# Performance work log

Measured on AMD Instinct MI355X. Metric: run time of the kernel, lower is better.

The kernel has to match this reference:

```python
import jax, jax.numpy as jnp
import numpy as np

BS, SLEN, EM = 32, 4096, 256


def setup_inputs() -> dict:
    key = jax.random.key(0)
    ks = jax.random.split(key, 8)
    word_embedded = jax.random.normal(ks[0], (BS, SLEN, EM), dtype=jnp.float32)
    # valid-token mask: first `length` tokens valid per row (True = keep)
    lengths = jax.random.randint(ks[1], (BS, 1), SLEN // 2, SLEN + 1)
    mask = jnp.arange(SLEN)[None, :] < lengths  # (BS, SLEN) bool
    s = 1.0 / np.sqrt(EM)
    w_query = jax.random.uniform(ks[2], (EM, 1), minval=-1.0, maxval=1.0, dtype=jnp.float32)  # Linear(1, em, bias=False)
    wq = jax.random.uniform(ks[3], (EM, EM), minval=-s, maxval=s, dtype=jnp.float32)
    bq = jax.random.uniform(ks[4], (EM,), minval=-s, maxval=s, dtype=jnp.float32)
    wk = jax.random.uniform(ks[5], (EM, EM), minval=-s, maxval=s, dtype=jnp.float32)
    bk = jax.random.uniform(ks[6], (EM,), minval=-s, maxval=s, dtype=jnp.float32)
    se = 1.0 / np.sqrt(2 * EM)
    we = jax.random.uniform(ks[7], (1, 2 * EM), minval=-se, maxval=se, dtype=jnp.float32)
    be = jnp.zeros((1,), dtype=jnp.float32)
    return {"word_embedded": word_embedded, "mask": mask, "w_query": w_query,
            "wq": wq, "bq": bq, "wk": wk, "bk": bk, "we": we, "be": be}


def reference(word_embedded, mask, w_query, wq, bq, wk, bk, we, be):
    bs, slen, em = word_embedded.shape
    # query = Linear(1, em, no bias) applied to ones -> each row is w_query[:, 0]
    q = jnp.broadcast_to(w_query[:, 0], (bs, em))          # (bs, em)
    qp = jax.nn.relu(q @ wq.T + bq)                        # (bs, em); dropout is identity at eval
    k = jax.nn.relu(word_embedded @ wk.T + bk)             # (bs, slen, em)
    # proj_e(tanh(cat(q, k))) == tanh(q)@we_q + tanh(k)@we_k + be (tanh is elementwise),
    # so we avoid materializing the (bs, slen, 2*em) concat.
    we_q, we_k = we[0, :em], we[0, em:]
    energy = jnp.tanh(qp) @ we_q                           # (bs,)
    energy = energy[:, None] + jnp.tanh(k) @ we_k + be[0]  # (bs, slen)
    # torch: energy.masked_fill_(~mask, 1e-45)
    energy = jnp.where(mask, energy, jnp.float32(1e-45))
    attn_weights = jax.nn.softmax(energy, axis=1)          # (bs, slen)
    sent_embedded = jnp.einsum('bs,bse->be', attn_weights, word_embedded)  # (bs, em)
    return sent_embedded
```

## Files before the change

### kernel.cpp

```cpp
#include <hip/hip_runtime.h>

#define BS   32
#define SLEN 4096
#define EM   256
#define NROWS (BS * SLEN)

typedef __attribute__((ext_vector_type(8))) short bf16x8;
typedef __attribute__((ext_vector_type(4))) float f32x4;

#define WS_WKB   0
#define WS_EN    32768
#define WS_CONST 163840
#define WS_W     163856
#define WS_PART  294928

__device__ inline short f2bf(float x) {
  union { float f; unsigned u; } v; v.f = x;
  unsigned r = v.u + 0x7fffu + ((v.u >> 16) & 1u);
  return (short)(r >> 16);
}

#define GLOAD_LDS16(g, l)                                                  \
  __builtin_amdgcn_global_load_lds(                                        \
      (const __attribute__((address_space(1))) unsigned int*)(g),          \
      (__attribute__((address_space(3))) unsigned int*)(l), 16, 0, 0)

__global__ __launch_bounds__(256) void k0_cvt(const float* __restrict__ wk,
                                              unsigned short* __restrict__ wkb2) {
  int gid = blockIdx.x * 256 + threadIdx.x;
  int e = gid >> 5, kq = gid & 31;
  const float* src = wk + (size_t)e * EM + kq * 8;
  float4 v0 = *(const float4*)src;
  float4 v1 = *(const float4*)(src + 4);
  bf16x8 pk;
  pk[0] = f2bf(v0.x); pk[1] = f2bf(v0.y); pk[2] = f2bf(v0.z); pk[3] = f2bf(v0.w);
  pk[4] = f2bf(v1.x); pk[5] = f2bf(v1.y); pk[6] = f2bf(v1.z); pk[7] = f2bf(v1.w);
  *(bf16x8*)(wkb2 + ((size_t)kq * 256 + e) * 8) = pk;
}

__global__ __launch_bounds__(256) void k0b_qscalar(const float* __restrict__ w_query,
                                                   const float* __restrict__ wq,
                                                   const float* __restrict__ bq,
                                                   const float* __restrict__ we,
                                                   const float* __restrict__ be,
                                                   float* __restrict__ outc) {
  int t = threadIdx.x;
  const float* row = wq + (size_t)t * EM;
  float4 a4 = make_float4(0.f, 0.f, 0.f, 0.f);
#pragma unroll 8
  for (int j = 0; j < 64; ++j) {
    float4 r = *(const float4*)(row + j * 4);
    float4 q = *(const float4*)(w_query + j * 4);
    a4.x = fmaf(r.x, q.x, a4.x);
    a4.y = fmaf(r.y, q.y, a4.y);
    a4.z = fmaf(r.z, q.z, a4.z);
    a4.w = fmaf(r.w, q.w, a4.w);
  }
  float a = (a4.x + a4.y) + (a4.z + a4.w) + bq[t];
  float kv = fmaxf(a, 0.f);
  float z = __expf(kv + kv);
  float v = we[t] * (1.f - __fdividef(2.f, z + 1.f));
#pragma unroll
  for (int off = 32; off >= 1; off >>= 1) v += __shfl_xor(v, off, 64);
  __shared__ float red[4];
  if ((t & 63) == 0) red[t >> 6] = v;
  __syncthreads();
  if (t == 0) outc[0] = red[0] + red[1] + red[2] + red[3] + be[0];
}

__global__ __launch_bounds__(256) void k1_energy(const float* __restrict__ X,
                                                 const unsigned short* __restrict__ wkb2,
                                                 const float* __restrict__ bk,
                                                 const float* __restrict__ we,
                                                 float* __restrict__ energy) {
  __shared__ char lds[41472];
  char* As = lds;
  char* Bs = lds + 8192;
  float* ep = (float*)(lds + 40960);
  const int tid = threadIdx.x;
  const int l = tid & 63;
  const int wid = tid >> 6;
  const int wr = wid >> 1, wc = wid & 1;
  const int lr = l & 15, lk = l >> 4;
  const int row0 = blockIdx.x * 64;
  const int ar = tid >> 2, ac = tid & 3;

  float bkv[8], wev[8];
#pragma unroll
  for (int n = 0; n < 8; ++n) {
    int e = wc * 128 + n * 16 + lr;
    bkv[n] = bk[e];
    wev[n] = we[EM + e];
  }
  f32x4 acc[2][8];
#pragma unroll
  for (int i = 0; i < 2; ++i)
#pragma unroll
    for (int n = 0; n < 8; ++n)
      acc[i][n] = (f32x4){bkv[n], bkv[n], bkv[n], bkv[n]};

#pragma unroll
  for (int q = 0; q < 4; ++q) {
    const char* g = (const char*)wkb2 + wid * 4096 + q * 1024 + l * 16;
    GLOAD_LDS16(g, Bs + wid * 4096 + q * 1024);
  }
  {
    const float* src = X + (size_t)(row0 + ar) * EM + ac * 8;
    float4 a0 = *(const float4*)src;
    float4 a1 = *(const float4*)(src + 4);
    bf16x8 pk;
    pk[0] = f2bf(a0.x); pk[1] = f2bf(a0.y); pk[2] = f2bf(a0.z); pk[3] = f2bf(a0.w);
    pk[4] = f2bf(a1.x); pk[5] = f2bf(a1.y); pk[6] = f2bf(a1.z); pk[7] = f2bf(a1.w);
    *(bf16x8*)(As + ar * 64 + ((ac ^ (ar & 3)) * 16)) = pk;
  }
  __syncthreads();

#pragma unroll
  for (int t = 0; t < 8; ++t) {
    const int cur = t & 1, nxt = cur ^ 1;
    float4 a0, a1;
    if (t < 7) {
#pragma unroll
      for (int q = 0; q < 4; ++q) {
        const char* g = (const char*)wkb2 + (t + 1) * 16384 + wid * 4096 + q * 1024 + l * 16;
        GLOAD_LDS16(g, Bs + nxt * 16384 + wid * 4096 + q * 1024);
      }
      const float* src = X + (size_t)(row0 + ar) * EM + (t + 1) * 32 + ac * 8;
      a0 = *(const float4*)src;
      a1 = *(const float4*)(src + 4);
    }
    bf16x8 af[2], bfr[8];
#pragma unroll
    for (int i = 0; i < 2; ++i) {
      int row = wr * 32 + i * 16 + lr;
      af[i] = *(const bf16x8*)(As + cur * 4096 + row * 64 + ((lk ^ (row & 3)) * 16));
    }
#pragma unroll
    for (int n = 0; n < 8; ++n)
      bfr[n] = *(const bf16x8*)(Bs + cur * 16384 + lk * 4096 + (wc * 128 + n * 16 + lr) * 16);
#pragma unroll
    for (int i = 0; i < 2; ++i)
#pragma unroll
      for (int n = 0; n < 8; ++n)
        acc[i][n] = __builtin_amdgcn_mfma_f32_16x16x32_bf16(af[i], bfr[n], acc[i][n], 0, 0, 0);
    if (t < 7) {
      bf16x8 pk;
      pk[0] = f2bf(a0.x); pk[1] = f2bf(a0.y); pk[2] = f2bf(a0.z); pk[3] = f2bf(a0.w);
      pk[4] = f2bf(a1.x); pk[5] = f2bf(a1.y); pk[6] = f2bf(a1.z); pk[7] = f2bf(a1.w);
      *(bf16x8*)(As + nxt * 4096 + ar * 64 + ((ac ^ (ar & 3)) * 16)) = pk;
    }
    __syncthreads();
  }

  float sumw = 0.f, w2[8];
#pragma unroll
  for (int n = 0; n < 8; ++n) { sumw += wev[n]; w2[n] = -2.f * wev[n]; }
#pragma unroll
  for (int i = 0; i < 2; ++i) {
#pragma unroll
    for (int r = 0; r < 4; ++r) {
      float p = sumw;
#pragma unroll
      for (int n = 0; n < 8; ++n) {
        float kv = fmaxf(acc[i][n][r], 0.f);
        float z = __expf(kv + kv);
        float rn = __fdividef(1.f, z + 1.f);
        p = fmaf(w2[n], rn, p);
      }
#pragma unroll
      for (int off = 1; off <= 8; off <<= 1) p += __shfl_xor(p, off, 64);
      if (lr == 0) ep[(wr * 32 + i * 16 + lk * 4 + r) * 2 + wc] = p;
    }
  }
  __syncthreads();
  if (tid < 64) energy[row0 + tid] = ep[tid * 2] + ep[tid * 2 + 1];
}

__global__ __launch_bounds__(256) void k2_softmax(const float* __restrict__ energy,
                                                  const unsigned char* __restrict__ mask,
                                                  const float* __restrict__ cptr,
                                                  float* __restrict__ wout) {
  const int b = blockIdx.x;
  const int t = threadIdx.x;
  const float C = cptr[0];
  const bool mask_is_byte = (mask[1] | mask[2] | mask[3]) != 0;
  const int* mask32 = (const int*)mask;
  const float* eb = energy + (size_t)b * SLEN;
  float v[16];
  float m = -3.4e38f;
#pragma unroll
  for (int i = 0; i < 16; ++i) {
    int s = t + i * 256;
    int mv = mask_is_byte ? (int)mask[(size_t)b * SLEN + s]
                          : mask32[(size_t)b * SLEN + s];
    float x = mv ? (eb[s] + C) : 1.4012984643248171e-45f;
    v[i] = x;
    m = fmaxf(m, x);
  }
  __shared__ float red[8];
#pragma unroll
  for (int off = 32; off >= 1; off >>= 1) m = fmaxf(m, __shfl_xor(m, off, 64));
  if ((t & 63) == 0) red[t >> 6] = m;
  __syncthreads();
  m = fmaxf(fmaxf(red[0], red[1]), fmaxf(red[2], red[3]));
  float s_ = 0.f;
#pragma unroll
  for (int i = 0; i < 16; ++i) {
    v[i] = __expf(v[i] - m);
    s_ += v[i];
  }
#pragma unroll
  for (int off = 32; off >= 1; off >>= 1) s_ += __shfl_xor(s_, off, 64);
  if ((t & 63) == 0) red[4 + (t >> 6)] = s_;
  __syncthreads();
  float inv = 1.f / (red[4] + red[5] + red[6] + red[7]);
  float* wb = wout + (size_t)b * SLEN;
#pragma unroll
  for (int i = 0; i < 16; ++i) wb[t + i * 256] = v[i] * inv;
}

__global__ __launch_bounds__(256) void k3_wsum(const float* __restrict__ X,
                                               const float* __restrict__ w,
                                               float* __restrict__ part) {
  __shared__ float red[4][EM];
  const int b = blockIdx.x >> 6;
  const int ch = blockIdx.x & 63;
  const int g = threadIdx.x >> 6;
  const int l = threadIdx.x & 63;
  const int s0 = ch * 64 + g * 16;
  const float* xb = X + (size_t)b * SLEN * EM;
  const float* wb = w + (size_t)b * SLEN;
  float4 acc = make_float4(0.f, 0.f, 0.f, 0.f);
#pragma unroll
  for (int i = 0; i < 16; ++i) {
    int s = s0 + i;
    float ws_ = wb[s];
    float4 v = *(const float4*)(xb + (size_t)s * EM + l * 4);
    acc.x = fmaf(ws_, v.x, acc.x);
    acc.y = fmaf(ws_, v.y, acc.y);
    acc.z = fmaf(ws_, v.z, acc.z);
    acc.w = fmaf(ws_, v.w, acc.w);
  }
  *(float4*)(&red[g][l * 4]) = acc;
  __syncthreads();
  if (g == 0) {
    float4 r0 = *(const float4*)(&red[0][l * 4]);
    float4 r1 = *(const float4*)(&red[1][l * 4]);
    float4 r2 = *(const float4*)(&red[2][l * 4]);
    float4 r3 = *(const float4*)(&red[3][l * 4]);
    float4 o;
    o.x = (r0.x + r1.x) + (r2.x + r3.x);
    o.y = (r0.y + r1.y) + (r2.y + r3.y);
    o.z = (r0.z + r1.z) + (r2.z + r3.z);
    o.w = (r0.w + r1.w) + (r2.w + r3.w);
    *(float4*)(part + (size_t)blockIdx.x * EM + l * 4) = o;
  }
}

__global__ __launch_bounds__(256) void k4_reduce(const float* __restrict__ part,
                                                 float* __restrict__ out) {
  const int b = blockIdx.x;
  const int e = threadIdx.x;
  float s = 0.f;
#pragma unroll 8
  for (int k = 0; k < 64; ++k) s += part[((size_t)b * 64 + k) * EM + e];
  out[(size_t)b * EM + e] = s;
}

extern "C" void kernel_launch(void* const* d_in, const int* in_sizes, int n_in,
                              void* d_out, int out_size, void* d_ws, size_t ws_size,
                              hipStream_t stream) {
  const float* X = (const float*)d_in[0];
  const unsigned char* mask = (const unsigned char*)d_in[1];
  const float* w_query = (const float*)d_in[2];
  const float* wq = (const float*)d_in[3];
  const float* bq = (const float*)d_in[4];
  const float* wk = (const float*)d_in[5];
  const float* bk = (const float*)d_in[6];
  const float* we = (const float*)d_in[7];
  const float* be = (const float*)d_in[8];
  float* out = (float*)d_out;
  float* ws = (float*)d_ws;

  unsigned short* wkb2 = (unsigned short*)(ws + WS_WKB);
  float* energy = ws + WS_EN;
  float* cscalar = ws + WS_CONST;
  float* weights = ws + WS_W;
  float* part = ws + WS_PART;

  k0_cvt<<<32, 256, 0, stream>>>(wk, wkb2);
  k0b_qscalar<<<1, 256, 0, stream>>>(w_query, wq, bq, we, be, cscalar);
  k1_energy<<<NROWS / 64, 256, 0, stream>>>(X, wkb2, bk, we, energy);
  k2_softmax<<<BS, 256, 0, stream>>>(energy, mask, cscalar, weights);
  k3_wsum<<<BS * 64, 256, 0, stream>>>(X, weights, part);
  k4_reduce<<<BS, 256, 0, stream>>>(part, out);
}
```

Baseline: 271.8 us.

## Keep full bf16 Wk in LDS and feed X directly from registers into MFMA

```diff
diff --git a/kernel.cpp b/kernel.cpp
--- a/kernel.cpp
+++ b/kernel.cpp
@@ -18,6 +18,20 @@
   union { float f; unsigned u; } v; v.f = x;
   unsigned r = v.u + 0x7fffu + ((v.u >> 16) & 1u);
   return (short)(r >> 16);
+}
+
+__device__ inline unsigned cvtpk(float lo, float hi) {
+  unsigned r;
+  asm("v_cvt_pk_bf16_f32 %0, %1, %2" : "=v"(r) : "v"(lo), "v"(hi));
+  return r;
+}
+__device__ inline bf16x8 cvt8(float4 a, float4 b) {
+  union { bf16x8 v; unsigned u[4]; } r;
+  r.u[0] = cvtpk(a.x, a.y);
+  r.u[1] = cvtpk(a.z, a.w);
+  r.u[2] = cvtpk(b.x, b.y);
+  r.u[3] = cvtpk(b.z, b.w);
+  return r.v;
 }
 
 #define GLOAD_LDS16(g, l)                                                  \
@@ -68,112 +82,86 @@
   if (t == 0) outc[0] = red[0] + red[1] + red[2] + red[3] + be[0];
 }
 
-__global__ __launch_bounds__(256) void k1_energy(const float* __restrict__ X,
+__global__ __launch_bounds__(512) void k1_energy(const float* __restrict__ X,
                                                  const unsigned short* __restrict__ wkb2,
                                                  const float* __restrict__ bk,
                                                  const float* __restrict__ we,
                                                  float* __restrict__ energy) {
-  __shared__ char lds[41472];
-  char* As = lds;
-  char* Bs = lds + 8192;
-  float* ep = (float*)(lds + 40960);
+  __shared__ char Bs[131072];
   const int tid = threadIdx.x;
   const int l = tid & 63;
-  const int wid = tid >> 6;
-  const int wr = wid >> 1, wc = wid & 1;
+  const int w = tid >> 6;
   const int lr = l & 15, lk = l >> 4;
-  const int row0 = blockIdx.x * 64;
-  const int ar = tid >> 2, ac = tid & 3;
-
-  float bkv[8], wev[8];
-#pragma unroll
-  for (int n = 0; n < 8; ++n) {
-    int e = wc * 128 + n * 16 + lr;
-    bkv[n] = bk[e];
-    wev[n] = we[EM + e];
-  }
-  f32x4 acc[2][8];
+  const int row0 = blockIdx.x * 256 + w * 32;
+
+#pragma unroll
+  for (int q = 0; q < 16; ++q) {
+    int seg = w * 16 + q;
+    GLOAD_LDS16((const char*)wkb2 + seg * 1024 + l * 16, Bs + seg * 1024);
+  }
+
+  float bkv[16], wev[16];
+#pragma unroll
+  for (int n = 0; n < 16; ++n) {
+    bkv[n] = bk[n * 16 + lr];
+    wev[n] = we[EM + n * 16 + lr];
+  }
+  f32x4 acc[2][16];
 #pragma unroll
   for (int i = 0; i < 2; ++i)
 #pragma unroll
-    for (int n = 0; n < 8; ++n)
+    for (int n = 0; n < 16; ++n)
       acc[i][n] = (f32x4){bkv[n], bkv[n], bkv[n], bkv[n]};
 
-#pragma unroll
-  for (int q = 0; q < 4; ++q) {
-    const char* g = (const char*)wkb2 + wid * 4096 + q * 1024 + l * 16;
-    GLOAD_LDS16(g, Bs + wid * 4096 + q * 1024);
-  }
-  {
-    const float* src = X + (size_t)(row0 + ar) * EM + ac * 8;
-    float4 a0 = *(const float4*)src;
-    float4 a1 = *(const float4*)(src + 4);
-    bf16x8 pk;
-    pk[0] = f2bf(a0.x); pk[1] = f2bf(a0.y); pk[2] = f2bf(a0.z); pk[3] = f2bf(a0.w);
-    pk[4] = f2bf(a1.x); pk[5] = f2bf(a1.y); pk[6] = f2bf(a1.z); pk[7] = f2bf(a1.w);
-    *(bf16x8*)(As + ar * 64 + ((ac ^ (ar & 3)) * 16)) = pk;
-  }
-  __syncthreads();
-
-#pragma unroll
-  for (int t = 0; t < 8; ++t) {
-    const int cur = t & 1, nxt = cur ^ 1;
-    float4 a0, a1;
-    if (t < 7) {
-#pragma unroll
-      for (int q = 0; q < 4; ++q) {
-        const char* g = (const char*)wkb2 + (t + 1) * 16384 + wid * 4096 + q * 1024 + l * 16;
-        GLOAD_LDS16(g, Bs + nxt * 16384 + wid * 4096 + q * 1024);
-      }
-      const float* src = X + (size_t)(row0 + ar) * EM + (t + 1) * 32 + ac * 8;
-      a0 = *(const float4*)src;
-      a1 = *(const float4*)(src + 4);
+  const float* xbase = X + (size_t)(row0 + lr) * EM + lk * 8;
+  float4 c00 = *(const float4*)(xbase);
+  float4 c01 = *(const float4*)(xbase + 4);
+  float4 c10 = *(const float4*)(xbase + 16 * EM);
+  float4 c11 = *(const float4*)(xbase + 16 * EM + 4);
+
+  __syncthreads();
+
+#pragma unroll
+  for (int s = 0; s < 8; ++s) {
+    float4 n00, n01, n10, n11;
+    if (s < 7) {
+      const float* nx = xbase + (s + 1) * 32;
+      n00 = *(const float4*)(nx);
+      n01 = *(const float4*)(nx + 4);
+      n10 = *(const float4*)(nx + 16 * EM);
+      n11 = *(const float4*)(nx + 16 * EM + 4);
     }
-    bf16x8 af[2], bfr[8];
-#pragma unroll
-    for (int i = 0; i < 2; ++i) {
-      int row = wr * 32 + i * 16 + lr;
-      af[i] = *(const bf16x8*)(As + cur * 4096 + row * 64 + ((lk ^ (row & 3)) * 16));
+    bf16x8 a0 = cvt8(c00, c01);
+    bf16x8 a1 = cvt8(c10, c11);
+    const char* bp = Bs + s * 16384 + lk * 4096 + lr * 16;
+#pragma unroll
+    for (int n = 0; n < 16; ++n) {
+      bf16x8 bfr = *(const bf16x8*)(bp + n * 256);
+      acc[0][n] = __builtin_amdgcn_mfma_f32_16x16x32_bf16(a0, bfr, acc[0][n], 0, 0, 0);
+      acc[1][n] = __builtin_amdgcn_mfma_f32_16x16x32_bf16(a1, bfr, acc[1][n], 0, 0, 0);
     }
-#pragma unroll
-    for (int n = 0; n < 8; ++n)
-      bfr[n] = *(const bf16x8*)(Bs + cur * 16384 + lk * 4096 + (wc * 128 + n * 16 + lr) * 16);
-#pragma unroll
-    for (int i = 0; i < 2; ++i)
-#pragma unroll
-      for (int n = 0; n < 8; ++n)
-        acc[i][n] = __builtin_amdgcn_mfma_f32_16x16x32_bf16(af[i], bfr[n], acc[i][n], 0, 0, 0);
-    if (t < 7) {
-      bf16x8 pk;
-      pk[0] = f2bf(a0.x); pk[1] = f2bf(a0.y); pk[2] = f2bf(a0.z); pk[3] = f2bf(a0.w);
-      pk[4] = f2bf(a1.x); pk[5] = f2bf(a1.y); pk[6] = f2bf(a1.z); pk[7] = f2bf(a1.w);
-      *(bf16x8*)(As + nxt * 4096 + ar * 64 + ((ac ^ (ar & 3)) * 16)) = pk;
-    }
-    __syncthreads();
-  }
-
-  float sumw = 0.f, w2[8];
-#pragma unroll
-  for (int n = 0; n < 8; ++n) { sumw += wev[n]; w2[n] = -2.f * wev[n]; }
+    c00 = n00; c01 = n01; c10 = n10; c11 = n11;
+  }
+
+  float sumw = 0.f, w2[16];
+#pragma unroll
+  for (int n = 0; n < 16; ++n) { sumw += wev[n]; w2[n] = -2.f * wev[n]; }
 #pragma unroll
   for (int i = 0; i < 2; ++i) {
 #pragma unroll
     for (int r = 0; r < 4; ++r) {
       float p = sumw;
 #pragma unroll
-      for (int n = 0; n < 8; ++n) {
+      for (int n = 0; n < 16; ++n) {
         float kv = fmaxf(acc[i][n][r], 0.f);
         float z = __expf(kv + kv);
-        float rn = __fdividef(1.f, z + 1.f);
-        p = fmaf(w2[n], rn, p);
+        p = fmaf(w2[n], __fdividef(1.f, z + 1.f), p);
       }
 #pragma unroll
-      for (int off = 1; off <= 8; off <<= 1) p += __shfl_xor(p, off, 64);
-      if (lr == 0) ep[(wr * 32 + i * 16 + lk * 4 + r) * 2 + wc] = p;
+      for (int off = 1; off <= 8; off <<= 1) p += __shfl_xor(p, off, 16);
+      if (lr == 0) energy[row0 + i * 16 + lk * 4 + r] = p;
     }
   }
-  __syncthreads();
-  if (tid < 64) energy[row0 + tid] = ep[tid * 2] + ep[tid * 2 + 1];
 }
 
 __global__ __launch_bounds__(256) void k2_softmax(const float* __restrict__ energy,
@@ -290,7 +278,7 @@
 
   k0_cvt<<<32, 256, 0, stream>>>(wk, wkb2);
   k0b_qscalar<<<1, 256, 0, stream>>>(w_query, wq, bq, we, be, cscalar);
-  k1_energy<<<NROWS / 64, 256, 0, stream>>>(X, wkb2, bk, we, energy);
+  k1_energy<<<NROWS / 256, 512, 0, stream>>>(X, wkb2, bk, we, energy);
   k2_softmax<<<BS, 256, 0, stream>>>(energy, mask, cscalar, weights);
   k3_wsum<<<BS * 64, 256, 0, stream>>>(X, weights, part);
   k4_reduce<<<BS, 256, 0, stream>>>(part, out);
```

After: 285.5 us. 5.0% more time.
